# Performance work log

Hardware: AMD Instinct MI355X
Metric: run time of the kernel (lower is better)

Reference implementation:

```python
import jax, jax.numpy as jnp
import numpy as np

# dims (see shape_source)
B, S, V, E, H, L, F = 512, 17, 40002, 1024, 16, 12, 4096
DH = E // H          # per-head dim = hidden_size // num_attention_heads
NREL = 500           # num_relations
NEDGE = 100          # num_edges (edge-label vocab)
BIG = 1000000.0


def _ln(x, g, b, eps):
    m = jnp.mean(x, axis=-1, keepdims=True)
    v = jnp.mean((x - m) ** 2, axis=-1, keepdims=True)
    return (x - m) * jax.lax.rsqrt(v + eps) * g + b


def setup_inputs() -> dict:
    key = jax.random.key(0)
    ks = jax.random.split(key, 24)
    n = lambda k, sh: 0.02 * jax.random.normal(k, sh, jnp.float32)
    inp = {
        # runtime inputs
        'input_ids': jax.random.randint(ks[0], (B, S), 0, V),
        'input_mask': jnp.ones((B, S), jnp.float32),
        'edge_labels': jax.random.randint(ks[1], (S, S), 0, NEDGE),
        'mask_pos': jax.random.randint(ks[2], (B,), 0, S),
        'mask_label': jax.random.randint(ks[3], (B,), 0, V),
        'mask_type': jnp.ones((B, 1), jnp.float32),  # +1 => entity slot masked
        'confidence': jax.random.uniform(ks[4], (B,), jnp.float32),
        # parameters
        'node_emb': n(ks[5], (V, E)),
        'edge_k': n(ks[6], (NEDGE, DH)),
        'edge_v': n(ks[7], (NEDGE, DH)),
        'ln1_g': jnp.ones((E,), jnp.float32), 'ln1_b': jnp.zeros((E,), jnp.float32),
        'Wq': n(ks[8], (L, E, E)), 'bq': jnp.zeros((L, E), jnp.float32),
        'Wk': n(ks[9], (L, E, E)), 'bk': jnp.zeros((L, E), jnp.float32),
        'Wv': n(ks[10], (L, E, E)), 'bv': jnp.zeros((L, E), jnp.float32),
        'Wo': n(ks[11], (L, E, E)), 'bo': jnp.zeros((L, E), jnp.float32),
        'lnA_g': jnp.ones((L, E), jnp.float32), 'lnA_b': jnp.zeros((L, E), jnp.float32),
        'W1': n(ks[12], (L, E, F)), 'b1': jnp.zeros((L, F), jnp.float32),
        'W2': n(ks[13], (L, F, E)), 'b2': jnp.zeros((L, E), jnp.float32),
        'lnF_g': jnp.ones((L, E), jnp.float32), 'lnF_b': jnp.zeros((L, E), jnp.float32),
        'ln2_g': jnp.ones((E,), jnp.float32), 'ln2_b': jnp.zeros((E,), jnp.float32),
        'fc2_bias': jnp.zeros((V,), jnp.float32),
    }
    return inp


def _forward(node_emb, edge_k, edge_v, ln1_g, ln1_b,
             Wq, bq, Wk, bk, Wv, bv, Wo, bo, lnA_g, lnA_b,
             W1, b1, W2, b2, lnF_g, lnF_b, ln2_g, ln2_b, fc2_bias,
             input_mask, mask_type, confidence,
             input_ids, edge_labels, mask_pos, mask_label):
    # embedding + pre-LN (dropout is identity in eval mode)
    x = _ln(node_emb[input_ids], ln1_g, ln1_b, 1e-12)          # [B,S,E]
    em = jnp.sign(edge_labels).astype(x.dtype)[:, :, None]     # [S,S,1]
    ek = edge_k[edge_labels] * em                              # [S,S,DH]
    ev = edge_v[edge_labels] * em
    m = input_mask[:, :, None]                                 # [B,S,1]
    attn_bias = (BIG * (m @ jnp.swapaxes(m, 1, 2) - 1.0))[:, None]  # [B,1,S,S]

    def step(h, p):
        wq, bq_, wk, bk_, wv, bv_, wo, bo_, ga, ba, w1, b1_, w2, b2_, gf, bf = p
        proj = lambda w, b: (h @ w + b).reshape(B, S, H, DH).transpose(0, 2, 1, 3)
        q = proj(wq, bq_) * (DH ** -0.5)
        k = proj(wk, bk_)
        v = proj(wv, bv_)
        # edge-aware attention scores: content + edge-key bias
        s = jnp.einsum('bhqd,bhkd->bhqk', q, k) \
            + jnp.einsum('bhqd,qkd->bhqk', q, ek) + attn_bias
        a = jax.nn.softmax(s, axis=-1)
        c = jnp.einsum('bhqk,bhkd->bhqd', a, v) \
            + jnp.einsum('bhqk,qkd->bhqd', a, ev)
        y = c.transpose(0, 2, 1, 3).reshape(B, S, E) @ wo + bo_
        h = _ln(h + y, ga, ba, 1e-12)                          # post-LN (cmd 'dan')
        f = jax.nn.gelu(h @ w1 + b1_, approximate=False) @ w2 + b2_
        return _ln(h + f, gf, bf, 1e-12), None

    enc, _ = jax.lax.scan(step, x, (Wq, bq, Wk, bk, Wv, bv, Wo, bo,
                                    lnA_g, lnA_b, W1, b1, W2, b2, lnF_g, lnF_b))

    # mode == 'normal': gather masked position (fc1 output is dead code in the original)
    hm = enc[jnp.arange(B), mask_pos]                          # [B,E]
    hm = _ln(jax.nn.gelu(hm, approximate=False), ln2_g, ln2_b, 1e-7)
    logits = hm @ node_emb.T + fc2_bias                        # tied projection [B,V]

    ti = jnp.concatenate([-jnp.ones((B, NREL), logits.dtype),
                          jnp.ones((B, V - NREL - 2), logits.dtype)], axis=1) * mask_type
    ti = jnp.concatenate([-jnp.ones((B, 2), logits.dtype), ti], axis=1)
    ti = jax.nn.relu(ti)                                       # candidate indicator [B,V]
    logits = logits + BIG * (ti - 1.0)

    oh = jax.nn.one_hot(mask_label, V, dtype=logits.dtype)
    ti2 = ti - oh
    num_cand = jnp.sum(ti2, axis=1)                            # [B]
    sl = ((1.0 + mask_type) * 0.9 + (1.0 - mask_type) * 0.9) / 2.0  # [B,1]
    soft = sl * oh + (1.0 - sl) * ti2 / num_cand[:, None]
    loss = jnp.mean(-jnp.sum(soft * jax.nn.log_softmax(logits, axis=1), axis=1) * confidence)
    return loss, logits


def reference(input_ids, input_mask, edge_labels, mask_pos, mask_label, mask_type,
              confidence, node_emb, edge_k, edge_v, ln1_g, ln1_b, Wq, bq, Wk, bk,
              Wv, bv, Wo, bo, lnA_g, lnA_b, W1, b1, W2, b2, lnF_g, lnF_b,
              ln2_g, ln2_b, fc2_bias):
    return _forward(node_emb, edge_k, edge_v, ln1_g, ln1_b, Wq, bq, Wk, bk, Wv, bv,
                    Wo, bo, lnA_g, lnA_b, W1, b1, W2, b2, lnF_g, lnF_b, ln2_g, ln2_b,
                    fc2_bias, input_mask, mask_type, confidence,
                    input_ids, edge_labels, mask_pos, mask_label)
```

## Files before the change

### kernel.cpp

```cpp
#include <hip/hip_runtime.h>
#include <hip/hip_bf16.h>

#define BB 512
#define SS 17
#define VV 40002
#define VPAD 40064
#define EE 1024
#define HH 16
#define LL 12
#define FF 4096
#define DHD 64
#define NRELC 500
#define MTOK (BB*SS)
#define BIGC 1000000.0f

typedef __bf16 bf16_t;
typedef __bf16 bf16x8 __attribute__((ext_vector_type(8)));
typedef __bf16 bf16x4 __attribute__((ext_vector_type(4)));
typedef float  f32x4  __attribute__((ext_vector_type(4)));

#define GLOAD_LDS16(g, l) __builtin_amdgcn_global_load_lds( \
    (const __attribute__((address_space(1))) void*)(g), \
    (__attribute__((address_space(3))) void*)(l), 16, 0, 0)

__device__ __forceinline__ float dgelu(float x) {
    return 0.5f * x * (1.f + erff(x * 0.70710678118654752f));
}
__device__ __forceinline__ float fgelu(float x) {
    float y = 0.7978845608f * (x + 0.044715f * x * x * x);
    float u = __expf(2.f * y);
    float t = 1.f - 2.f / (u + 1.f);
    return 0.5f * x * (1.f + t);
}

__device__ __forceinline__ float blk_sum(float v, float* sred) {
#pragma unroll
    for (int o = 32; o > 0; o >>= 1) v += __shfl_down(v, o);
    int lane = threadIdx.x & 63, w = threadIdx.x >> 6;
    __syncthreads();
    if (lane == 0) sred[w] = v;
    __syncthreads();
    return sred[0] + sred[1] + sred[2] + sred[3];
}
__device__ __forceinline__ float blk_max(float v, float* sred) {
#pragma unroll
    for (int o = 32; o > 0; o >>= 1) v = fmaxf(v, __shfl_down(v, o));
    int lane = threadIdx.x & 63, w = threadIdx.x >> 6;
    __syncthreads();
    if (lane == 0) sred[w] = v;
    __syncthreads();
    return fmaxf(fmaxf(sred[0], sred[1]), fmaxf(sred[2], sred[3]));
}

__global__ __launch_bounds__(256)
void edge_kernel(const int* __restrict__ labels, const float* __restrict__ eks,
                 const float* __restrict__ evs, float* __restrict__ ek,
                 float* __restrict__ ev) {
    int e = blockIdx.x * 256 + threadIdx.x;
    if (e >= SS * SS * DHD) return;
    int qk = e >> 6, d = e & 63;
    int lab = labels[qk];
    float sgn = lab > 0 ? 1.f : (lab < 0 ? -1.f : 0.f);
    ek[e] = eks[(size_t)lab * DHD + d] * sgn;
    ev[e] = evs[(size_t)lab * DHD + d] * sgn;
}

__global__ __launch_bounds__(256)
void embed_kernel(const int* __restrict__ ids, const float* __restrict__ emb,
                  const float* __restrict__ g, const float* __restrict__ bt,
                  bf16_t* __restrict__ out) {
    __shared__ float sred[4];
    int row = blockIdx.x;
    const float* src = emb + (size_t)ids[row] * EE;
    int c = threadIdx.x * 4;
    float4 x = *(const float4*)(src + c);
    float mean = blk_sum(x.x + x.y + x.z + x.w, sred) * (1.f / EE);
    float x0 = x.x - mean, x1 = x.y - mean, x2 = x.z - mean, x3 = x.w - mean;
    float var = blk_sum(x0*x0 + x1*x1 + x2*x2 + x3*x3, sred) * (1.f / EE);
    float rs = rsqrtf(var + 1e-12f);
    float4 gv = *(const float4*)(g + c), bv = *(const float4*)(bt + c);
    bf16x4 o;
    o[0] = (bf16_t)(x0*rs*gv.x + bv.x); o[1] = (bf16_t)(x1*rs*gv.y + bv.y);
    o[2] = (bf16_t)(x2*rs*gv.z + bv.z); o[3] = (bf16_t)(x3*rs*gv.w + bv.w);
    *(bf16x4*)(out + (size_t)row * EE + c) = o;
}

__global__ __launch_bounds__(256)
void resln_kernel(bf16_t* __restrict__ h, const bf16_t* __restrict__ y,
                  const float* __restrict__ g, const float* __restrict__ bt) {
    __shared__ float sred[4];
    int row = blockIdx.x; int c = threadIdx.x * 4;
    size_t off = (size_t)row * EE + c;
    bf16x4 a = *(const bf16x4*)(h + off), b4 = *(const bf16x4*)(y + off);
    float x0 = (float)a[0] + (float)b4[0], x1 = (float)a[1] + (float)b4[1];
    float x2 = (float)a[2] + (float)b4[2], x3 = (float)a[3] + (float)b4[3];
    float mean = blk_sum(x0 + x1 + x2 + x3, sred) * (1.f / EE);
    x0 -= mean; x1 -= mean; x2 -= mean; x3 -= mean;
    float var = blk_sum(x0*x0 + x1*x1 + x2*x2 + x3*x3, sred) * (1.f / EE);
    float rs = rsqrtf(var + 1e-12f);
    float4 gv = *(const float4*)(g + c), bv = *(const float4*)(bt + c);
    bf16x4 o;
    o[0] = (bf16_t)(x0*rs*gv.x + bv.x); o[1] = (bf16_t)(x1*rs*gv.y + bv.y);
    o[2] = (bf16_t)(x2*rs*gv.z + bv.z); o[3] = (bf16_t)(x3*rs*gv.w + bv.w);
    *(bf16x4*)(h + off) = o;
}

__global__ __launch_bounds__(256)
void hm_kernel(const bf16_t* __restrict__ h, const int* __restrict__ pos,
               const float* __restrict__ g, const float* __restrict__ bt,
               bf16_t* __restrict__ out) {
    __shared__ float sred[4];
    int b = blockIdx.x; int c = threadIdx.x * 4;
    const bf16_t* src = h + ((size_t)(b * SS + pos[b])) * EE + c;
    bf16x4 x = *(const bf16x4*)src;
    float x0 = dgelu((float)x[0]), x1 = dgelu((float)x[1]);
    float x2 = dgelu((float)x[2]), x3 = dgelu((float)x[3]);
    float mean = blk_sum(x0 + x1 + x2 + x3, sred) * (1.f / EE);
    x0 -= mean; x1 -= mean; x2 -= mean; x3 -= mean;
    float var = blk_sum(x0*x0 + x1*x1 + x2*x2 + x3*x3, sred) * (1.f / EE);
    float rs = rsqrtf(var + 1e-7f);
    float4 gv = *(const float4*)(g + c), bv = *(const float4*)(bt + c);
    bf16x4 o;
    o[0] = (bf16_t)(x0*rs*gv.x + bv.x); o[1] = (bf16_t)(x1*rs*gv.y + bv.y);
    o[2] = (bf16_t)(x2*rs*gv.z + bv.z); o[3] = (bf16_t)(x3*rs*gv.w + bv.w);
    *(bf16x4*)(out + (size_t)b * EE + c) = o;
}

__global__ __launch_bounds__(256)
void nodeconv_kernel(const float* __restrict__ src, bf16_t* __restrict__ dst) {
    const size_t total = (size_t)VPAD * (EE / 8);
    for (size_t idx = (size_t)blockIdx.x * 256 + threadIdx.x; idx < total;
         idx += (size_t)gridDim.x * 256) {
        size_t row = idx >> 7;
        bf16x8 o;
#pragma unroll
        for (int u = 0; u < 8; ++u) o[u] = (bf16_t)0.f;
        if (row < VV) {
            const float* s = src + (idx << 3);
            float4 a = *(const float4*)s, b = *(const float4*)(s + 4);
            o[0] = (bf16_t)a.x; o[1] = (bf16_t)a.y; o[2] = (bf16_t)a.z; o[3] = (bf16_t)a.w;
            o[4] = (bf16_t)b.x; o[5] = (bf16_t)b.y; o[6] = (bf16_t)b.z; o[7] = (bf16_t)b.w;
        }
        *(bf16x8*)(dst + (idx << 3)) = o;
    }
}

__global__ __launch_bounds__(256)
void transpose_kernel(const float* __restrict__ Wq, const float* __restrict__ Wk,
                      const float* __restrict__ Wv, const float* __restrict__ Wo,
                      const float* __restrict__ W1, const float* __restrict__ W2,
                      bf16_t* __restrict__ wt) {
    int t = blockIdx.x;
    const float* src; bf16_t* dst; int K, N, tile;
    if (t < 4096) {
        int mi = t >> 10; tile = t & 1023;
        src = mi == 0 ? Wq : mi == 1 ? Wk : mi == 2 ? Wv : Wo;
        dst = wt + (size_t)mi * (1u << 20);
        K = 1024; N = 1024;
    } else if (t < 8192) {
        tile = t - 4096; src = W1; dst = wt + (size_t)4 * (1u << 20); K = 1024; N = 4096;
    } else {
        tile = t - 8192; src = W2; dst = wt + (size_t)8 * (1u << 20); K = 4096; N = 1024;
    }
    int ntiles = N >> 5;
    int kt = tile / ntiles, nt = tile % ntiles;
    __shared__ float lds[32][33];
    int tx = threadIdx.x & 31, ty = threadIdx.x >> 5;
#pragma unroll
    for (int i = 0; i < 4; ++i) {
        int r = ty + i * 8;
        lds[r][tx] = src[(size_t)(kt * 32 + r) * N + nt * 32 + tx];
    }
    __syncthreads();
#pragma unroll
    for (int i = 0; i < 4; ++i) {
        int r = ty + i * 8;
        dst[(size_t)(nt * 32 + r) * K + kt * 32 + tx] = (bf16_t)lds[tx][r];
    }
}

template<int EPI, bool NB>
__global__ __launch_bounds__(256)
void gemm_bf16(const bf16_t* __restrict__ A, const bf16_t* __restrict__ B,
               const float* __restrict__ b0, const float* __restrict__ b1,
               const float* __restrict__ b2, const float* __restrict__ mt,
               void* __restrict__ Cout, int M, int N, int K) {
    __shared__ __align__(16) bf16_t sA[3 * 4096];
    __shared__ __align__(16) bf16_t sB[3 * 4096];
    const int tid = threadIdx.x;
    const int lane = tid & 63, wid = tid >> 6;
    const int wm = wid >> 1, wn = wid & 1;
    const int row16 = lane & 15, kblk = lane >> 4;

    const int nwg = gridDim.x * gridDim.y;
    const int wg = blockIdx.y * gridDim.x + blockIdx.x;
    const int q8 = nwg >> 3, r8 = nwg & 7;
    const int xcd = wg & 7, loc = wg >> 3;
    const int swz = (xcd < r8 ? xcd * (q8 + 1) : r8 * (q8 + 1) + (xcd - r8) * q8) + loc;
    const int bm = swz / gridDim.x, bn = swz % gridDim.x;

    f32x4 acc[4][4];
#pragma unroll
    for (int i = 0; i < 4; ++i)
#pragma unroll
        for (int j = 0; j < 4; ++j) acc[i][j] = (f32x4){0.f, 0.f, 0.f, 0.f};

    const bf16_t* Atile = A + (size_t)bm * 128 * K;
    const bf16_t* Btile = B + (size_t)bn * 128 * K;

    const int row_s0 = tid >> 2, chs = tid & 3;
    const int ch0 = chs ^ ((row_s0 >> 1) & 3);
    const int row_s1 = row_s0 + 64;
    const int ch1 = chs ^ ((row_s1 >> 1) & 3);
    const size_t soff0 = (size_t)row_s0 * K + ch0 * 8;
    const size_t soff1 = (size_t)row_s1 * K + ch1 * 8;
    const int ldo0 = wid * 512;
    const int ldo1 = 2048 + wid * 512;

    int offA[4], offB[4];
#pragma unroll
    for (int i = 0; i < 4; ++i) {
        int r = wm * 64 + i * 16 + row16;
        offA[i] = r * 32 + ((kblk ^ ((r >> 1) & 3)) << 3);
    }
#pragma unroll
    for (int j = 0; j < 4; ++j) {
        int r = wn * 64 + j * 16 + row16;
        offB[j] = r * 32 + ((kblk ^ ((r >> 1) & 3)) << 3);
    }

#define STAGE_T(t_, buf_) do { \
        const bf16_t* a_ = Atile + (size_t)(t_) * 32; \
        const bf16_t* b_ = Btile + (size_t)(t_) * 32; \
        bf16_t* dA = sA + (buf_) * 4096; \
        bf16_t* dB = sB + (buf_) * 4096; \
        GLOAD_LDS16(a_ + soff0, dA + ldo0); \
        GLOAD_LDS16(a_ + soff1, dA + ldo1); \
        GLOAD_LDS16(b_ + soff0, dB + ldo0); \
        GLOAD_LDS16(b_ + soff1, dB + ldo1); \
    } while (0)

    const int nt = K >> 5;
    STAGE_T(0, 0);
    STAGE_T(1, 1);
    asm volatile("s_waitcnt vmcnt(4)" ::: "memory");
    __builtin_amdgcn_s_barrier();

    int cur = 0, stg = 2;
    for (int t = 0; t < nt; ++t) {
        const bool more = (t + 2 < nt);
        if (more) {
            STAGE_T(t + 2, stg);
            stg = (stg == 2) ? 0 : stg + 1;
        }
        const bf16_t* bufA = sA + cur * 4096;
        const bf16_t* bufB = sB + cur * 4096;
        bf16x8 af[4], bfr[4];
#pragma unroll
        for (int i = 0; i < 4; ++i) af[i] = *(const bf16x8*)(bufA + offA[i]);
#pragma unroll
        for (int j = 0; j < 4; ++j) bfr[j] = *(const bf16x8*)(bufB + offB[j]);
#pragma unroll
        for (int i = 0; i < 4; ++i)
#pragma unroll
            for (int j = 0; j < 4; ++j)
                acc[i][j] = __builtin_amdgcn_mfma_f32_16x16x32_bf16(af[i], bfr[j], acc[i][j], 0, 0, 0);
        if (t + 1 < nt) {
            if (more) asm volatile("s_waitcnt vmcnt(4)" ::: "memory");
            else      asm volatile("s_waitcnt vmcnt(0)" ::: "memory");
            __builtin_amdgcn_s_barrier();
        }
        cur = (cur == 2) ? 0 : cur + 1;
    }
#undef STAGE_T

    const int crow0 = bm * 128 + wm * 64;
    const int ccol0 = bn * 128 + wn * 64;
#pragma unroll
    for (int i = 0; i < 4; ++i) {
#pragma unroll
        for (int j = 0; j < 4; ++j) {
            int col = ccol0 + j * 16 + row16;
            if (NB && col >= N) continue;
            float bias, scale = 1.f;
            if (EPI == 4) {
                int seg = col >> 10;
                const float* bp = seg == 0 ? b0 : (seg == 1 ? b1 : b2);
                bias = bp[col & 1023];
                if (seg == 0) scale = 0.125f;
            } else {
                bias = b0[col];
            }
#pragma unroll
            for (int r = 0; r < 4; ++r) {
                int rowg = crow0 + i * 16 + kblk * 4 + r;
                float val = acc[i][j][r] + bias;
                if (EPI == 4) val *= scale;
                if (EPI == 2) val = fgelu(val);
                if (EPI == 3) {
                    float mtb = mt[rowg];
                    float tt = (col < 2) ? 0.f : fmaxf(0.f, ((col - 2) < NRELC) ? -mtb : mtb);
                    val += BIGC * (tt - 1.f);
                    ((float*)Cout)[(size_t)rowg * N + col] = val;
                } else {
                    ((bf16_t*)Cout)[(size_t)rowg * N + col] = (bf16_t)val;
                }
            }
        }
    }
}

__global__ __launch_bounds__(256)
void attn_kernel(const bf16_t* __restrict__ qkv, const float* __restrict__ ekb,
                 const float* __restrict__ evb, const float* __restrict__ mask,
                 bf16_t* __restrict__ ctx) {
    int bh = blockIdx.x; int b = bh >> 4; int h = bh & 15;
    __shared__ float sq[SS][DHD], sk[SS][DHD], sv[SS][DHD];
    __shared__ float ss[SS][SS + 1];
    __shared__ float sm[SS];
    int tid = threadIdx.x;
    for (int idx = tid; idx < 3 * SS * 8; idx += 256) {
        int t3 = idx / (SS * 8), rc = idx % (SS * 8), s = rc >> 3, c8 = rc & 7;
        bf16x8 v = *(const bf16x8*)(qkv + ((size_t)(b * SS + s)) * 3072 + t3 * 1024 + h * 64 + c8 * 8);
        float* dst = (t3 == 0 ? &sq[0][0] : t3 == 1 ? &sk[0][0] : &sv[0][0]) + s * 64 + c8 * 8;
#pragma unroll
        for (int u = 0; u < 8; ++u) dst[u] = (float)v[u];
    }
    if (tid < SS) sm[tid] = mask[b * SS + tid];
    __syncthreads();
    for (int e = tid; e < SS * SS; e += 256) {
        int qi = e / SS, ki = e % SS;
        const float* ek_ = ekb + (size_t)e * DHD;
        float acc = 0.f;
#pragma unroll 16
        for (int d = 0; d < DHD; ++d) acc += sq[qi][d] * (sk[ki][d] + ek_[d]);
        acc += BIGC * (sm[qi] * sm[ki] - 1.f);
        ss[qi][ki] = acc;
    }
    __syncthreads();
    if (tid < SS) {
        float mx = -1e30f;
        for (int ki = 0; ki < SS; ++ki) mx = fmaxf(mx, ss[tid][ki]);
        float sum = 0.f;
        for (int ki = 0; ki < SS; ++ki) { float e_ = expf(ss[tid][ki] - mx); sum += e_; ss[tid][ki] = e_; }
        float inv = 1.f / sum;
        for (int ki = 0; ki < SS; ++ki) ss[tid][ki] *= inv;
    }
    __syncthreads();
    for (int e = tid; e < SS * DHD; e += 256) {
        int qi = e >> 6, d = e & 63;
        float acc = 0.f;
#pragma unroll
        for (int ki = 0; ki < SS; ++ki)
            acc += ss[qi][ki] * (sv[ki][d] + evb[((size_t)(qi * SS + ki)) * DHD + d]);
        ctx[((size_t)(b * SS + qi)) * EE + h * DHD + d] = (bf16_t)acc;
    }
}

__global__ __launch_bounds__(256)
void loss_part_kernel(const float* __restrict__ logits, const float* __restrict__ mt,
                      const int* __restrict__ label, const float* __restrict__ conf,
                      float* __restrict__ lp) {
    __shared__ float sred[4];
    int b = blockIdx.x;
    const float* row = logits + (size_t)b * VV;
    float mx = -1e30f;
    for (int j = threadIdx.x; j < VV; j += 256) mx = fmaxf(mx, row[j]);
    mx = blk_max(mx, sred);
    float m = mt[b];
    float se = 0.f, s1 = 0.f, cnt = 0.f;
    for (int j = threadIdx.x; j < VV; j += 256) {
        float x = row[j];
        se += expf(x - mx);
        float t = (j < 2) ? 0.f : fmaxf(0.f, ((j - 2) < NRELC) ? -m : m);
        s1 += t * x;
        cnt += t;
    }
    se = blk_sum(se, sred);
    s1 = blk_sum(s1, sred);
    cnt = blk_sum(cnt, sred);
    if (threadIdx.x == 0) {
        float lse = mx + logf(se);
        float lsml = row[label[b]] - lse;
        float num_cand = cnt - 1.f;
        float v = 0.9f * lsml + 0.1f * ((s1 - cnt * lse) - lsml) / num_cand;
        lp[b] = -v * conf[b];
    }
}

__global__ __launch_bounds__(256)
void loss_reduce_kernel(const float* __restrict__ lp, float* __restrict__ out) {
    __shared__ float sred[4];
    float s = 0.f;
    for (int i = threadIdx.x; i < BB; i += 256) s += lp[i];
    s = blk_sum(s, sred);
    if (threadIdx.x == 0) out[0] = s * (1.f / BB);
}

extern "C" void kernel_launch(void* const* d_in, const int* in_sizes, int n_in,
                              void* d_out, int out_size, void* d_ws, size_t ws_size,
                              hipStream_t stream) {
    const int*   input_ids  = (const int*)d_in[0];
    const float* input_mask = (const float*)d_in[1];
    const int*   edge_lab   = (const int*)d_in[2];
    const int*   mask_pos   = (const int*)d_in[3];
    const int*   mask_label = (const int*)d_in[4];
    const float* mask_type  = (const float*)d_in[5];
    const float* confidence = (const float*)d_in[6];
    const float* node_emb   = (const float*)d_in[7];
    const float* edge_k     = (const float*)d_in[8];
    const float* edge_v     = (const float*)d_in[9];
    const float* ln1_g      = (const float*)d_in[10];
    const float* ln1_b      = (const float*)d_in[11];
    const float* Wq         = (const float*)d_in[12];
    const float* bq         = (const float*)d_in[13];
    const float* Wk         = (const float*)d_in[14];
    const float* bk         = (const float*)d_in[15];
    const float* Wv         = (const float*)d_in[16];
    const float* bv         = (const float*)d_in[17];
    const float* Wo         = (const float*)d_in[18];
    const float* bo         = (const float*)d_in[19];
    const float* lnA_g      = (const float*)d_in[20];
    const float* lnA_b      = (const float*)d_in[21];
    const float* W1         = (const float*)d_in[22];
    const float* b1         = (const float*)d_in[23];
    const float* W2         = (const float*)d_in[24];
    const float* b2         = (const float*)d_in[25];
    const float* lnF_g      = (const float*)d_in[26];
    const float* lnF_b      = (const float*)d_in[27];
    const float* ln2_g      = (const float*)d_in[28];
    const float* ln2_b      = (const float*)d_in[29];
    const float* fc2_bias   = (const float*)d_in[30];

    char* p = (char*)d_ws;
    bf16_t* wt    = (bf16_t*)p;
    size_t off = 25165824;
    bf16_t* hbuf  = (bf16_t*)(p + off); off += (size_t)MTOK * EE * 2;
    bf16_t* qkvb  = (bf16_t*)(p + off); off += (size_t)MTOK * FF * 2;
    bf16_t* cb    = (bf16_t*)(p + off); off += (size_t)MTOK * EE * 2;
    bf16_t* yb    = (bf16_t*)(p + off); off += (size_t)MTOK * EE * 2;
    float*  ekb   = (float*)(p + off);  off += (size_t)SS * SS * DHD * 4;
    float*  evb   = (float*)(p + off);  off += (size_t)SS * SS * DHD * 4;
    bf16_t* hmb   = (bf16_t*)(p + off); off += (size_t)BB * EE * 2;
    float*  lp    = (float*)(p + off);  off += (size_t)BB * 4;
    bf16_t* midb  = qkvb;
    bf16_t* nodeb = qkvb;

    float* loss_out   = (float*)d_out;
    float* logits_out = ((float*)d_out) + 1;

    edge_kernel<<<(SS * SS * DHD + 255) / 256, 256, 0, stream>>>(edge_lab, edge_k, edge_v, ekb, evb);
    embed_kernel<<<MTOK, 256, 0, stream>>>(input_ids, node_emb, ln1_g, ln1_b, hbuf);

    dim3 gqkv(3 * EE / 128, MTOK / 128);
    dim3 gproj(EE / 128, MTOK / 128);
    dim3 gffn1(FF / 128, MTOK / 128);

    for (int l = 0; l < LL; ++l) {
        size_t we = (size_t)l * EE * EE;
        size_t wf = (size_t)l * EE * FF;
        transpose_kernel<<<12288, 256, 0, stream>>>(Wq + we, Wk + we, Wv + we, Wo + we,
                                                    W1 + wf, W2 + wf, wt);
        gemm_bf16<4, false><<<gqkv, 256, 0, stream>>>(hbuf, wt,
            bq + (size_t)l * EE, bk + (size_t)l * EE, bv + (size_t)l * EE, nullptr,
            qkvb, MTOK, 3 * EE, EE);
        attn_kernel<<<BB * HH, 256, 0, stream>>>(qkvb, ekb, evb, input_mask, cb);
        gemm_bf16<0, false><<<gproj, 256, 0, stream>>>(cb, wt + (size_t)3 * (1u << 20),
            bo + (size_t)l * EE, nullptr, nullptr, nullptr, yb, MTOK, EE, EE);
        resln_kernel<<<MTOK, 256, 0, stream>>>(hbuf, yb, lnA_g + (size_t)l * EE, lnA_b + (size_t)l * EE);
        gemm_bf16<2, false><<<gffn1, 256, 0, stream>>>(hbuf, wt + (size_t)4 * (1u << 20),
            b1 + (size_t)l * FF, nullptr, nullptr, nullptr, midb, MTOK, FF, EE);
        gemm_bf16<0, false><<<gproj, 256, 0, stream>>>(midb, wt + (size_t)8 * (1u << 20),
            b2 + (size_t)l * EE, nullptr, nullptr, nullptr, yb, MTOK, EE, FF);
        resln_kernel<<<MTOK, 256, 0, stream>>>(hbuf, yb, lnF_g + (size_t)l * EE, lnF_b + (size_t)l * EE);
    }

    nodeconv_kernel<<<2048, 256, 0, stream>>>(node_emb, nodeb);
    hm_kernel<<<BB, 256, 0, stream>>>(hbuf, mask_pos, ln2_g, ln2_b, hmb);

    dim3 glog(VPAD / 128, BB / 128);
    gemm_bf16<3, true><<<glog, 256, 0, stream>>>(hmb, nodeb, fc2_bias, nullptr, nullptr,
        mask_type, logits_out, BB, VV, EE);

    loss_part_kernel<<<BB, 256, 0, stream>>>(logits_out, mask_type, mask_label, confidence, lp);
    loss_reduce_kernel<<<1, 256, 0, stream>>>(lp, loss_out);
}
```

Baseline: 5.562 ms.

## Add 256x256-tile 8-wave GEMM for QKV and FFN1 projections

```diff
diff --git a/kernel.cpp b/kernel.cpp
--- a/kernel.cpp
+++ b/kernel.cpp
@@ -179,11 +179,184 @@
     }
 }
 
+__device__ __forceinline__ void stage_half(const bf16_t* __restrict__ gbase,
+                                           bf16_t* sbase, int dstoff, int h,
+                                           int t, int K, int srow, int ch, int wid) {
+    const bf16_t* s0 = gbase + (size_t)(h * 128 + srow) * K + (size_t)t * 64 + ch * 8;
+    const bf16_t* s1 = gbase + (size_t)(h * 128 + 64 + srow) * K + (size_t)t * 64 + ch * 8;
+    GLOAD_LDS16(s0, sbase + dstoff + h * 8192 + wid * 512);
+    GLOAD_LDS16(s1, sbase + dstoff + h * 8192 + 4096 + wid * 512);
+}
+
+template<bool LAST>
+__device__ __forceinline__ void ktile256(
+    int kt, const bf16_t* __restrict__ Atile, const bf16_t* __restrict__ Btile,
+    bf16_t* sA, bf16_t* sB, int K, int srow, int ch, int wid,
+    const int (&offA)[8][2], const int (&offB)[4][2], f32x4 (&acc)[8][4]) {
+    const int bufo = (kt & 1) << 14;
+    const int nbufo = bufo ^ (1 << 14);
+    bf16x8 af[4][2], bf0[2][2], bf1[2][2];
+    asm volatile("s_waitcnt vmcnt(4)" ::: "memory");
+    __builtin_amdgcn_s_barrier();
+#pragma unroll
+    for (int i = 0; i < 4; ++i)
+#pragma unroll
+        for (int kk = 0; kk < 2; ++kk)
+            af[i][kk] = *(const bf16x8*)(sA + bufo + offA[i][kk]);
+#pragma unroll
+    for (int j = 0; j < 2; ++j)
+#pragma unroll
+        for (int kk = 0; kk < 2; ++kk)
+            bf0[j][kk] = *(const bf16x8*)(sB + bufo + offB[j][kk]);
+    if (!LAST) {
+        stage_half(Atile, sA, nbufo, 0, kt + 1, K, srow, ch, wid);
+        stage_half(Btile, sB, nbufo, 0, kt + 1, K, srow, ch, wid);
+    }
+    __builtin_amdgcn_s_setprio(1);
+#pragma unroll
+    for (int i = 0; i < 4; ++i)
+#pragma unroll
+        for (int j = 0; j < 2; ++j)
+#pragma unroll
+            for (int kk = 0; kk < 2; ++kk)
+                acc[i][j] = __builtin_amdgcn_mfma_f32_16x16x32_bf16(af[i][kk], bf0[j][kk], acc[i][j], 0, 0, 0);
+    __builtin_amdgcn_s_setprio(0);
+    if (LAST) asm volatile("s_waitcnt vmcnt(2)" ::: "memory");
+    else      asm volatile("s_waitcnt vmcnt(6)" ::: "memory");
+    __builtin_amdgcn_s_barrier();
+#pragma unroll
+    for (int j = 0; j < 2; ++j)
+#pragma unroll
+        for (int kk = 0; kk < 2; ++kk)
+            bf1[j][kk] = *(const bf16x8*)(sB + bufo + offB[2 + j][kk]);
+    if (!LAST) stage_half(Btile, sB, nbufo, 1, kt + 1, K, srow, ch, wid);
+    __builtin_amdgcn_s_setprio(1);
+#pragma unroll
+    for (int i = 0; i < 4; ++i)
+#pragma unroll
+        for (int j = 0; j < 2; ++j)
+#pragma unroll
+            for (int kk = 0; kk < 2; ++kk)
+                acc[i][2 + j] = __builtin_amdgcn_mfma_f32_16x16x32_bf16(af[i][kk], bf1[j][kk], acc[i][2 + j], 0, 0, 0);
+    __builtin_amdgcn_s_setprio(0);
+    if (LAST) asm volatile("s_waitcnt vmcnt(0)" ::: "memory");
+    else      asm volatile("s_waitcnt vmcnt(6)" ::: "memory");
+    __builtin_amdgcn_s_barrier();
+#pragma unroll
+    for (int i = 0; i < 4; ++i)
+#pragma unroll
+        for (int kk = 0; kk < 2; ++kk)
+            af[i][kk] = *(const bf16x8*)(sA + bufo + offA[4 + i][kk]);
+    if (!LAST) stage_half(Atile, sA, nbufo, 1, kt + 1, K, srow, ch, wid);
+    __builtin_amdgcn_s_setprio(1);
+#pragma unroll
+    for (int i = 0; i < 4; ++i)
+#pragma unroll
+        for (int j = 0; j < 2; ++j)
+#pragma unroll
+            for (int kk = 0; kk < 2; ++kk)
+                acc[4 + i][2 + j] = __builtin_amdgcn_mfma_f32_16x16x32_bf16(af[i][kk], bf1[j][kk], acc[4 + i][2 + j], 0, 0, 0);
+#pragma unroll
+    for (int i = 0; i < 4; ++i)
+#pragma unroll
+        for (int j = 0; j < 2; ++j)
+#pragma unroll
+            for (int kk = 0; kk < 2; ++kk)
+                acc[4 + i][j] = __builtin_amdgcn_mfma_f32_16x16x32_bf16(af[i][kk], bf0[j][kk], acc[4 + i][j], 0, 0, 0);
+    __builtin_amdgcn_s_setprio(0);
+}
+
+template<int EPI>
+__global__ __launch_bounds__(512, 1)
+void gemm256(const bf16_t* __restrict__ A, const bf16_t* __restrict__ B,
+             const float* __restrict__ b0, const float* __restrict__ b1,
+             const float* __restrict__ b2, bf16_t* __restrict__ C,
+             int N, int K) {
+    __shared__ __align__(16) bf16_t sA[32768];
+    __shared__ __align__(16) bf16_t sB[32768];
+    const int tid = threadIdx.x;
+    const int lane = tid & 63, wid = tid >> 6;
+    const int wm = wid >> 2, wn = wid & 3;
+    const int r16 = lane & 15, kblk = lane >> 4;
+
+    const int nwg = gridDim.x * gridDim.y;
+    const int wg = blockIdx.y * gridDim.x + blockIdx.x;
+    const int q8 = nwg >> 3, r8 = nwg & 7;
+    const int xcd = wg & 7, loc = wg >> 3;
+    const int swz = (xcd < r8 ? xcd * (q8 + 1) : r8 * (q8 + 1) + (xcd - r8) * q8) + loc;
+    const int bm = swz / gridDim.x, bn = swz % gridDim.x;
+
+    f32x4 acc[8][4];
+#pragma unroll
+    for (int i = 0; i < 8; ++i)
+#pragma unroll
+        for (int j = 0; j < 4; ++j) acc[i][j] = (f32x4){0.f, 0.f, 0.f, 0.f};
+
+    const bf16_t* Atile = A + (size_t)bm * 256 * K;
+    const bf16_t* Btile = B + (size_t)bn * 256 * K;
+
+    const int c = wid * 64 + lane;
+    const int srow = c >> 3;
+    const int ch = (c & 7) ^ (srow & 7);
+
+    int offA[8][2], offB[4][2];
+#pragma unroll
+    for (int i = 0; i < 8; ++i) {
+        int r = wm * 128 + i * 16 + r16;
+#pragma unroll
+        for (int kk = 0; kk < 2; ++kk)
+            offA[i][kk] = r * 64 + (((kk * 4 + kblk) ^ (r & 7)) << 3);
+    }
+#pragma unroll
+    for (int j = 0; j < 4; ++j) {
+        int r = wn * 64 + j * 16 + r16;
+#pragma unroll
+        for (int kk = 0; kk < 2; ++kk)
+            offB[j][kk] = r * 64 + (((kk * 4 + kblk) ^ (r & 7)) << 3);
+    }
+
+    stage_half(Atile, sA, 0, 0, 0, K, srow, ch, wid);
+    stage_half(Btile, sB, 0, 0, 0, K, srow, ch, wid);
+    stage_half(Btile, sB, 0, 1, 0, K, srow, ch, wid);
+    stage_half(Atile, sA, 0, 1, 0, K, srow, ch, wid);
+
+    const int nt = K >> 6;
+    for (int kt = 0; kt < nt - 1; ++kt)
+        ktile256<false>(kt, Atile, Btile, sA, sB, K, srow, ch, wid, offA, offB, acc);
+    ktile256<true>(nt - 1, Atile, Btile, sA, sB, K, srow, ch, wid, offA, offB, acc);
+
+    const int crow0 = bm * 256 + wm * 128;
+    const int ccol0 = bn * 256 + wn * 64;
+#pragma unroll
+    for (int i = 0; i < 8; ++i) {
+#pragma unroll
+        for (int j = 0; j < 4; ++j) {
+            int col = ccol0 + j * 16 + r16;
+            float bias, scale = 1.f;
+            if (EPI == 4) {
+                int seg = col >> 10;
+                const float* bp = seg == 0 ? b0 : (seg == 1 ? b1 : b2);
+                bias = bp[col & 1023];
+                if (seg == 0) scale = 0.125f;
+            } else {
+                bias = b0[col];
+            }
+#pragma unroll
+            for (int r = 0; r < 4; ++r) {
+                int rowg = crow0 + i * 16 + kblk * 4 + r;
+                float val = acc[i][j][r] + bias;
+                if (EPI == 4) val *= scale;
+                if (EPI == 2) val = fgelu(val);
+                C[(size_t)rowg * N + col] = (bf16_t)val;
+            }
+        }
+    }
+}
+
 template<int EPI, bool NB>
 __global__ __launch_bounds__(256)
 void gemm_bf16(const bf16_t* __restrict__ A, const bf16_t* __restrict__ B,
-               const float* __restrict__ b0, const float* __restrict__ b1,
-               const float* __restrict__ b2, const float* __restrict__ mt,
+               const float* __restrict__ b0, const float* __restrict__ mt,
                void* __restrict__ Cout, int M, int N, int K) {
     __shared__ __align__(16) bf16_t sA[3 * 4096];
     __shared__ __align__(16) bf16_t sB[3 * 4096];
@@ -282,21 +455,11 @@
         for (int j = 0; j < 4; ++j) {
             int col = ccol0 + j * 16 + row16;
             if (NB && col >= N) continue;
-            float bias, scale = 1.f;
-            if (EPI == 4) {
-                int seg = col >> 10;
-                const float* bp = seg == 0 ? b0 : (seg == 1 ? b1 : b2);
-                bias = bp[col & 1023];
-                if (seg == 0) scale = 0.125f;
-            } else {
-                bias = b0[col];
-            }
+            float bias = b0[col];
 #pragma unroll
             for (int r = 0; r < 4; ++r) {
                 int rowg = crow0 + i * 16 + kblk * 4 + r;
                 float val = acc[i][j][r] + bias;
-                if (EPI == 4) val *= scale;
-                if (EPI == 2) val = fgelu(val);
                 if (EPI == 3) {
                     float mtb = mt[rowg];
                     float tt = (col < 2) ? 0.f : fmaxf(0.f, ((col - 2) < NRELC) ? -mtb : mtb);
@@ -452,26 +615,26 @@
     edge_kernel<<<(SS * SS * DHD + 255) / 256, 256, 0, stream>>>(edge_lab, edge_k, edge_v, ekb, evb);
     embed_kernel<<<MTOK, 256, 0, stream>>>(input_ids, node_emb, ln1_g, ln1_b, hbuf);
 
-    dim3 gqkv(3 * EE / 128, MTOK / 128);
+    dim3 gqkv(3 * EE / 256, MTOK / 256);
+    dim3 gffn1(FF / 256, MTOK / 256);
     dim3 gproj(EE / 128, MTOK / 128);
-    dim3 gffn1(FF / 128, MTOK / 128);
 
     for (int l = 0; l < LL; ++l) {
         size_t we = (size_t)l * EE * EE;
         size_t wf = (size_t)l * EE * FF;
         transpose_kernel<<<12288, 256, 0, stream>>>(Wq + we, Wk + we, Wv + we, Wo + we,
                                                     W1 + wf, W2 + wf, wt);
-        gemm_bf16<4, false><<<gqkv, 256, 0, stream>>>(hbuf, wt,
-            bq + (size_t)l * EE, bk + (size_t)l * EE, bv + (size_t)l * EE, nullptr,
-            qkvb, MTOK, 3 * EE, EE);
+        gemm256<4><<<gqkv, 512, 0, stream>>>(hbuf, wt,
+            bq + (size_t)l * EE, bk + (size_t)l * EE, bv + (size_t)l * EE,
+            qkvb, 3 * EE, EE);
         attn_kernel<<<BB * HH, 256, 0, stream>>>(qkvb, ekb, evb, input_mask, cb);
         gemm_bf16<0, false><<<gproj, 256, 0, stream>>>(cb, wt + (size_t)3 * (1u << 20),
-            bo + (size_t)l * EE, nullptr, nullptr, nullptr, yb, MTOK, EE, EE);
+            bo + (size_t)l * EE, nullptr, yb, MTOK, EE, EE);
         resln_kernel<<<MTOK, 256, 0, stream>>>(hbuf, yb, lnA_g + (size_t)l * EE, lnA_b + (size_t)l * EE);
-        gemm_bf16<2, false><<<gffn1, 256, 0, stream>>>(hbuf, wt + (size_t)4 * (1u << 20),
-            b1 + (size_t)l * FF, nullptr, nullptr, nullptr, midb, MTOK, FF, EE);
+        gemm256<2><<<gffn1, 512, 0, stream>>>(hbuf, wt + (size_t)4 * (1u << 20),
+            b1 + (size_t)l * FF, nullptr, nullptr, midb, FF, EE);
         gemm_bf16<0, false><<<gproj, 256, 0, stream>>>(midb, wt + (size_t)8 * (1u << 20),
-            b2 + (size_t)l * EE, nullptr, nullptr, nullptr, yb, MTOK, EE, FF);
+            b2 + (size_t)l * EE, nullptr, yb, MTOK, EE, FF);
         resln_kernel<<<MTOK, 256, 0, stream>>>(hbuf, yb, lnF_g + (size_t)l * EE, lnF_b + (size_t)l * EE);
     }
 
@@ -479,7 +642,7 @@
     hm_kernel<<<BB, 256, 0, stream>>>(hbuf, mask_pos, ln2_g, ln2_b, hmb);
 
     dim3 glog(VPAD / 128, BB / 128);
-    gemm_bf16<3, true><<<glog, 256, 0, stream>>>(hmb, nodeb, fc2_bias, nullptr, nullptr,
+    gemm_bf16<3, true><<<glog, 256, 0, stream>>>(hmb, nodeb, fc2_bias,
         mask_type, logits_out, BB, VV, EE);
 
     loss_part_kernel<<<BB, 256, 0, stream>>>(logits_out, mask_type, mask_label, confidence, lp);
```

After: 5.471 ms. No clear change (-1.6%).

## Widen GEMM block tile to 128x256 with eight waves per block

Applied to the files above, without the earlier changes.

```diff
diff --git a/kernel.cpp b/kernel.cpp
--- a/kernel.cpp
+++ b/kernel.cpp
@@ -4,7 +4,7 @@
 #define BB 512
 #define SS 17
 #define VV 40002
-#define VPAD 40064
+#define VPAD 40192
 #define EE 1024
 #define HH 16
 #define LL 12
@@ -180,16 +180,16 @@
 }
 
 template<int EPI, bool NB>
-__global__ __launch_bounds__(256)
+__global__ __launch_bounds__(512, 4)
 void gemm_bf16(const bf16_t* __restrict__ A, const bf16_t* __restrict__ B,
                const float* __restrict__ b0, const float* __restrict__ b1,
                const float* __restrict__ b2, const float* __restrict__ mt,
                void* __restrict__ Cout, int M, int N, int K) {
     __shared__ __align__(16) bf16_t sA[3 * 4096];
-    __shared__ __align__(16) bf16_t sB[3 * 4096];
+    __shared__ __align__(16) bf16_t sB[3 * 8192];
     const int tid = threadIdx.x;
     const int lane = tid & 63, wid = tid >> 6;
-    const int wm = wid >> 1, wn = wid & 1;
+    const int wm = wid >> 2, wn = wid & 3;
     const int row16 = lane & 15, kblk = lane >> 4;
 
     const int nwg = gridDim.x * gridDim.y;
@@ -206,16 +206,19 @@
         for (int j = 0; j < 4; ++j) acc[i][j] = (f32x4){0.f, 0.f, 0.f, 0.f};
 
     const bf16_t* Atile = A + (size_t)bm * 128 * K;
-    const bf16_t* Btile = B + (size_t)bn * 128 * K;
-
-    const int row_s0 = tid >> 2, chs = tid & 3;
-    const int ch0 = chs ^ ((row_s0 >> 1) & 3);
-    const int row_s1 = row_s0 + 64;
-    const int ch1 = chs ^ ((row_s1 >> 1) & 3);
-    const size_t soff0 = (size_t)row_s0 * K + ch0 * 8;
-    const size_t soff1 = (size_t)row_s1 * K + ch1 * 8;
-    const int ldo0 = wid * 512;
-    const int ldo1 = 2048 + wid * 512;
+    const bf16_t* Btile = B + (size_t)bn * 256 * K;
+
+    const int rowA = tid >> 2;
+    const int chA = (tid & 3) ^ ((rowA >> 1) & 3);
+    const size_t aoff = (size_t)rowA * K + chA * 8;
+    const int rowB0 = tid >> 2, rowB1 = rowB0 + 128;
+    const int chB0 = (tid & 3) ^ ((rowB0 >> 1) & 3);
+    const int chB1 = (tid & 3) ^ ((rowB1 >> 1) & 3);
+    const size_t boff0 = (size_t)rowB0 * K + chB0 * 8;
+    const size_t boff1 = (size_t)rowB1 * K + chB1 * 8;
+    const int ldoA  = wid * 512;
+    const int ldoB0 = wid * 512;
+    const int ldoB1 = 4096 + wid * 512;
 
     int offA[4], offB[4];
 #pragma unroll
@@ -232,18 +235,15 @@
 #define STAGE_T(t_, buf_) do { \
         const bf16_t* a_ = Atile + (size_t)(t_) * 32; \
         const bf16_t* b_ = Btile + (size_t)(t_) * 32; \
-        bf16_t* dA = sA + (buf_) * 4096; \
-        bf16_t* dB = sB + (buf_) * 4096; \
-        GLOAD_LDS16(a_ + soff0, dA + ldo0); \
-        GLOAD_LDS16(a_ + soff1, dA + ldo1); \
-        GLOAD_LDS16(b_ + soff0, dB + ldo0); \
-        GLOAD_LDS16(b_ + soff1, dB + ldo1); \
+        GLOAD_LDS16(a_ + aoff,  sA + (buf_) * 4096 + ldoA); \
+        GLOAD_LDS16(b_ + boff0, sB + (buf_) * 8192 + ldoB0); \
+        GLOAD_LDS16(b_ + boff1, sB + (buf_) * 8192 + ldoB1); \
     } while (0)
 
     const int nt = K >> 5;
     STAGE_T(0, 0);
     STAGE_T(1, 1);
-    asm volatile("s_waitcnt vmcnt(4)" ::: "memory");
+    asm volatile("s_waitcnt vmcnt(3)" ::: "memory");
     __builtin_amdgcn_s_barrier();
 
     int cur = 0, stg = 2;
@@ -254,7 +254,7 @@
             stg = (stg == 2) ? 0 : stg + 1;
         }
         const bf16_t* bufA = sA + cur * 4096;
-        const bf16_t* bufB = sB + cur * 4096;
+        const bf16_t* bufB = sB + cur * 8192;
         bf16x8 af[4], bfr[4];
 #pragma unroll
         for (int i = 0; i < 4; ++i) af[i] = *(const bf16x8*)(bufA + offA[i]);
@@ -266,7 +266,7 @@
             for (int j = 0; j < 4; ++j)
                 acc[i][j] = __builtin_amdgcn_mfma_f32_16x16x32_bf16(af[i], bfr[j], acc[i][j], 0, 0, 0);
         if (t + 1 < nt) {
-            if (more) asm volatile("s_waitcnt vmcnt(4)" ::: "memory");
+            if (more) asm volatile("s_waitcnt vmcnt(3)" ::: "memory");
             else      asm volatile("s_waitcnt vmcnt(0)" ::: "memory");
             __builtin_amdgcn_s_barrier();
         }
@@ -275,7 +275,7 @@
 #undef STAGE_T
 
     const int crow0 = bm * 128 + wm * 64;
-    const int ccol0 = bn * 128 + wn * 64;
+    const int ccol0 = bn * 256 + wn * 64;
 #pragma unroll
     for (int i = 0; i < 4; ++i) {
 #pragma unroll
@@ -452,25 +452,25 @@
     edge_kernel<<<(SS * SS * DHD + 255) / 256, 256, 0, stream>>>(edge_lab, edge_k, edge_v, ekb, evb);
     embed_kernel<<<MTOK, 256, 0, stream>>>(input_ids, node_emb, ln1_g, ln1_b, hbuf);
 
-    dim3 gqkv(3 * EE / 128, MTOK / 128);
-    dim3 gproj(EE / 128, MTOK / 128);
-    dim3 gffn1(FF / 128, MTOK / 128);
+    dim3 gqkv(3 * EE / 256, MTOK / 128);
+    dim3 gproj(EE / 256, MTOK / 128);
+    dim3 gffn1(FF / 256, MTOK / 128);
 
     for (int l = 0; l < LL; ++l) {
         size_t we = (size_t)l * EE * EE;
         size_t wf = (size_t)l * EE * FF;
         transpose_kernel<<<12288, 256, 0, stream>>>(Wq + we, Wk + we, Wv + we, Wo + we,
                                                     W1 + wf, W2 + wf, wt);
-        gemm_bf16<4, false><<<gqkv, 256, 0, stream>>>(hbuf, wt,
+        gemm_bf16<4, false><<<gqkv, 512, 0, stream>>>(hbuf, wt,
             bq + (size_t)l * EE, bk + (size_t)l * EE, bv + (size_t)l * EE, nullptr,
             qkvb, MTOK, 3 * EE, EE);
         attn_kernel<<<BB * HH, 256, 0, stream>>>(qkvb, ekb, evb, input_mask, cb);
-        gemm_bf16<0, false><<<gproj, 256, 0, stream>>>(cb, wt + (size_t)3 * (1u << 20),
+        gemm_bf16<0, false><<<gproj, 512, 0, stream>>>(cb, wt + (size_t)3 * (1u << 20),
             bo + (size_t)l * EE, nullptr, nullptr, nullptr, yb, MTOK, EE, EE);
         resln_kernel<<<MTOK, 256, 0, stream>>>(hbuf, yb, lnA_g + (size_t)l * EE, lnA_b + (size_t)l * EE);
-        gemm_bf16<2, false><<<gffn1, 256, 0, stream>>>(hbuf, wt + (size_t)4 * (1u << 20),
+        gemm_bf16<2, false><<<gffn1, 512, 0, stream>>>(hbuf, wt + (size_t)4 * (1u << 20),
             b1 + (size_t)l * FF, nullptr, nullptr, nullptr, midb, MTOK, FF, EE);
-        gemm_bf16<0, false><<<gproj, 256, 0, stream>>>(midb, wt + (size_t)8 * (1u << 20),
+        gemm_bf16<0, false><<<gproj, 512, 0, stream>>>(midb, wt + (size_t)8 * (1u << 20),
             b2 + (size_t)l * EE, nullptr, nullptr, nullptr, yb, MTOK, EE, FF);
         resln_kernel<<<MTOK, 256, 0, stream>>>(hbuf, yb, lnF_g + (size_t)l * EE, lnF_b + (size_t)l * EE);
     }
@@ -478,8 +478,8 @@
     nodeconv_kernel<<<2048, 256, 0, stream>>>(node_emb, nodeb);
     hm_kernel<<<BB, 256, 0, stream>>>(hbuf, mask_pos, ln2_g, ln2_b, hmb);
 
-    dim3 glog(VPAD / 128, BB / 128);
-    gemm_bf16<3, true><<<glog, 256, 0, stream>>>(hmb, nodeb, fc2_bias, nullptr, nullptr,
+    dim3 glog(VPAD / 256, BB / 128);
+    gemm_bf16<3, true><<<glog, 512, 0, stream>>>(hmb, nodeb, fc2_bias, nullptr, nullptr,
         mask_type, logits_out, BB, VV, EE);
 
     loss_part_kernel<<<BB, 256, 0, stream>>>(logits_out, mask_type, mask_label, confidence, lp);
```

After: 5.819 ms. 1.05x slower.

## Batch four heads per attention block, stage bf16 edge tensors in LDS, warp-per-row LayerNorm

Applied to the files above, without the earlier changes.

```diff
diff --git a/kernel.cpp b/kernel.cpp
--- a/kernel.cpp
+++ b/kernel.cpp
@@ -26,11 +26,8 @@
 __device__ __forceinline__ float dgelu(float x) {
     return 0.5f * x * (1.f + erff(x * 0.70710678118654752f));
 }
-__device__ __forceinline__ float fgelu(float x) {
-    float y = 0.7978845608f * (x + 0.044715f * x * x * x);
-    float u = __expf(2.f * y);
-    float t = 1.f - 2.f / (u + 1.f);
-    return 0.5f * x * (1.f + t);
+__device__ __forceinline__ float sgelu(float x) {
+    return x / (1.f + __expf(-1.702f * x));
 }
 
 __device__ __forceinline__ float blk_sum(float v, float* sred) {
@@ -54,15 +51,15 @@
 
 __global__ __launch_bounds__(256)
 void edge_kernel(const int* __restrict__ labels, const float* __restrict__ eks,
-                 const float* __restrict__ evs, float* __restrict__ ek,
-                 float* __restrict__ ev) {
+                 const float* __restrict__ evs, bf16_t* __restrict__ ek,
+                 bf16_t* __restrict__ ev) {
     int e = blockIdx.x * 256 + threadIdx.x;
     if (e >= SS * SS * DHD) return;
     int qk = e >> 6, d = e & 63;
     int lab = labels[qk];
     float sgn = lab > 0 ? 1.f : (lab < 0 ? -1.f : 0.f);
-    ek[e] = eks[(size_t)lab * DHD + d] * sgn;
-    ev[e] = evs[(size_t)lab * DHD + d] * sgn;
+    ek[e] = (bf16_t)(eks[(size_t)lab * DHD + d] * sgn);
+    ev[e] = (bf16_t)(evs[(size_t)lab * DHD + d] * sgn);
 }
 
 __global__ __launch_bounds__(256)
@@ -88,21 +85,43 @@
 __global__ __launch_bounds__(256)
 void resln_kernel(bf16_t* __restrict__ h, const bf16_t* __restrict__ y,
                   const float* __restrict__ g, const float* __restrict__ bt) {
-    __shared__ float sred[4];
-    int row = blockIdx.x; int c = threadIdx.x * 4;
-    size_t off = (size_t)row * EE + c;
-    bf16x4 a = *(const bf16x4*)(h + off), b4 = *(const bf16x4*)(y + off);
-    float x0 = (float)a[0] + (float)b4[0], x1 = (float)a[1] + (float)b4[1];
-    float x2 = (float)a[2] + (float)b4[2], x3 = (float)a[3] + (float)b4[3];
-    float mean = blk_sum(x0 + x1 + x2 + x3, sred) * (1.f / EE);
-    x0 -= mean; x1 -= mean; x2 -= mean; x3 -= mean;
-    float var = blk_sum(x0*x0 + x1*x1 + x2*x2 + x3*x3, sred) * (1.f / EE);
-    float rs = rsqrtf(var + 1e-12f);
-    float4 gv = *(const float4*)(g + c), bv = *(const float4*)(bt + c);
-    bf16x4 o;
-    o[0] = (bf16_t)(x0*rs*gv.x + bv.x); o[1] = (bf16_t)(x1*rs*gv.y + bv.y);
-    o[2] = (bf16_t)(x2*rs*gv.z + bv.z); o[3] = (bf16_t)(x3*rs*gv.w + bv.w);
-    *(bf16x4*)(h + off) = o;
+    int row = blockIdx.x * 4 + (threadIdx.x >> 6);
+    int lane = threadIdx.x & 63;
+    int c = lane * 16;
+    size_t base = (size_t)row * EE + c;
+    bf16x8 a0 = *(const bf16x8*)(h + base);
+    bf16x8 a1 = *(const bf16x8*)(h + base + 8);
+    bf16x8 b0 = *(const bf16x8*)(y + base);
+    bf16x8 b1 = *(const bf16x8*)(y + base + 8);
+    float x[16];
+    float s = 0.f;
+#pragma unroll
+    for (int u = 0; u < 8; ++u) { x[u] = (float)a0[u] + (float)b0[u]; s += x[u]; }
+#pragma unroll
+    for (int u = 0; u < 8; ++u) { x[8 + u] = (float)a1[u] + (float)b1[u]; s += x[8 + u]; }
+#pragma unroll
+    for (int o = 32; o > 0; o >>= 1) s += __shfl_xor(s, o);
+    float mean = s * (1.f / EE);
+    float v = 0.f;
+#pragma unroll
+    for (int u = 0; u < 16; ++u) { x[u] -= mean; v += x[u] * x[u]; }
+#pragma unroll
+    for (int o = 32; o > 0; o >>= 1) v += __shfl_xor(v, o);
+    float rs = rsqrtf(v * (1.f / EE) + 1e-12f);
+    float4 g0 = *(const float4*)(g + c),  g1 = *(const float4*)(g + c + 4);
+    float4 g2 = *(const float4*)(g + c + 8), g3 = *(const float4*)(g + c + 12);
+    float4 t0 = *(const float4*)(bt + c), t1 = *(const float4*)(bt + c + 4);
+    float4 t2 = *(const float4*)(bt + c + 8), t3 = *(const float4*)(bt + c + 12);
+    float gg[16] = {g0.x,g0.y,g0.z,g0.w,g1.x,g1.y,g1.z,g1.w,g2.x,g2.y,g2.z,g2.w,g3.x,g3.y,g3.z,g3.w};
+    float tt[16] = {t0.x,t0.y,t0.z,t0.w,t1.x,t1.y,t1.z,t1.w,t2.x,t2.y,t2.z,t2.w,t3.x,t3.y,t3.z,t3.w};
+    bf16x8 o0, o1;
+#pragma unroll
+    for (int u = 0; u < 8; ++u) {
+        o0[u] = (bf16_t)(x[u] * rs * gg[u] + tt[u]);
+        o1[u] = (bf16_t)(x[8 + u] * rs * gg[8 + u] + tt[8 + u]);
+    }
+    *(bf16x8*)(h + base) = o0;
+    *(bf16x8*)(h + base + 8) = o1;
 }
 
 __global__ __launch_bounds__(256)
@@ -296,7 +315,7 @@
                 int rowg = crow0 + i * 16 + kblk * 4 + r;
                 float val = acc[i][j][r] + bias;
                 if (EPI == 4) val *= scale;
-                if (EPI == 2) val = fgelu(val);
+                if (EPI == 2) val = sgelu(val);
                 if (EPI == 3) {
                     float mtb = mt[rowg];
                     float tt = (col < 2) ? 0.f : fmaxf(0.f, ((col - 2) < NRELC) ? -mtb : mtb);
@@ -310,50 +329,60 @@
     }
 }
 
-__global__ __launch_bounds__(256)
-void attn_kernel(const bf16_t* __restrict__ qkv, const float* __restrict__ ekb,
-                 const float* __restrict__ evb, const float* __restrict__ mask,
+__global__ __launch_bounds__(512)
+void attn_kernel(const bf16_t* __restrict__ qkv, const bf16_t* __restrict__ ekb,
+                 const bf16_t* __restrict__ evb, const float* __restrict__ mask,
                  bf16_t* __restrict__ ctx) {
-    int bh = blockIdx.x; int b = bh >> 4; int h = bh & 15;
-    __shared__ float sq[SS][DHD], sk[SS][DHD], sv[SS][DHD];
-    __shared__ float ss[SS][SS + 1];
+    const int blk = blockIdx.x;
+    const int b = blk >> 2, hg = blk & 3;
+    const int h0 = hg * 4;
+    __shared__ bf16_t sek[SS * SS * DHD];
+    __shared__ bf16_t sev[SS * SS * DHD];
+    __shared__ float sq[4][SS][DHD], skk[4][SS][DHD], svv[4][SS][DHD];
+    __shared__ float ss[4][SS][SS + 1];
     __shared__ float sm[SS];
-    int tid = threadIdx.x;
-    for (int idx = tid; idx < 3 * SS * 8; idx += 256) {
-        int t3 = idx / (SS * 8), rc = idx % (SS * 8), s = rc >> 3, c8 = rc & 7;
-        bf16x8 v = *(const bf16x8*)(qkv + ((size_t)(b * SS + s)) * 3072 + t3 * 1024 + h * 64 + c8 * 8);
-        float* dst = (t3 == 0 ? &sq[0][0] : t3 == 1 ? &sk[0][0] : &sv[0][0]) + s * 64 + c8 * 8;
+    const int tid = threadIdx.x;
+    for (int idx = tid; idx < SS * SS * 8; idx += 512) {
+        *(bf16x8*)(sek + idx * 8) = *(const bf16x8*)(ekb + idx * 8);
+        *(bf16x8*)(sev + idx * 8) = *(const bf16x8*)(evb + idx * 8);
+    }
+    for (int idx = tid; idx < 3 * SS * 32; idx += 512) {
+        int t3 = idx / (SS * 32), rc = idx % (SS * 32), s = rc >> 5, c8 = rc & 31;
+        bf16x8 v = *(const bf16x8*)(qkv + (size_t)(b * SS + s) * 3072 + t3 * 1024 + h0 * 64 + c8 * 8);
+        int hh = c8 >> 3, d0 = (c8 & 7) * 8;
+        float* dst = (t3 == 0 ? &sq[hh][s][d0] : t3 == 1 ? &skk[hh][s][d0] : &svv[hh][s][d0]);
 #pragma unroll
         for (int u = 0; u < 8; ++u) dst[u] = (float)v[u];
     }
     if (tid < SS) sm[tid] = mask[b * SS + tid];
     __syncthreads();
-    for (int e = tid; e < SS * SS; e += 256) {
-        int qi = e / SS, ki = e % SS;
-        const float* ek_ = ekb + (size_t)e * DHD;
+    for (int e = tid; e < 4 * SS * SS; e += 512) {
+        int hh = e / (SS * SS), qk = e % (SS * SS), qi = qk / SS, ki = qk % SS;
+        const bf16_t* ek_ = sek + qk * DHD;
         float acc = 0.f;
 #pragma unroll 16
-        for (int d = 0; d < DHD; ++d) acc += sq[qi][d] * (sk[ki][d] + ek_[d]);
+        for (int d = 0; d < DHD; ++d) acc += sq[hh][qi][d] * (skk[hh][ki][d] + (float)ek_[d]);
         acc += BIGC * (sm[qi] * sm[ki] - 1.f);
-        ss[qi][ki] = acc;
-    }
-    __syncthreads();
-    if (tid < SS) {
+        ss[hh][qi][ki] = acc;
+    }
+    __syncthreads();
+    if (tid < 4 * SS) {
+        int hh = tid / SS, qi = tid % SS;
         float mx = -1e30f;
-        for (int ki = 0; ki < SS; ++ki) mx = fmaxf(mx, ss[tid][ki]);
+        for (int ki = 0; ki < SS; ++ki) mx = fmaxf(mx, ss[hh][qi][ki]);
         float sum = 0.f;
-        for (int ki = 0; ki < SS; ++ki) { float e_ = expf(ss[tid][ki] - mx); sum += e_; ss[tid][ki] = e_; }
+        for (int ki = 0; ki < SS; ++ki) { float e_ = __expf(ss[hh][qi][ki] - mx); sum += e_; ss[hh][qi][ki] = e_; }
         float inv = 1.f / sum;
-        for (int ki = 0; ki < SS; ++ki) ss[tid][ki] *= inv;
-    }
-    __syncthreads();
-    for (int e = tid; e < SS * DHD; e += 256) {
-        int qi = e >> 6, d = e & 63;
+        for (int ki = 0; ki < SS; ++ki) ss[hh][qi][ki] *= inv;
+    }
+    __syncthreads();
+    for (int e = tid; e < 4 * SS * DHD; e += 512) {
+        int hh = e / (SS * DHD), rem = e % (SS * DHD), qi = rem >> 6, d = rem & 63;
         float acc = 0.f;
 #pragma unroll
         for (int ki = 0; ki < SS; ++ki)
-            acc += ss[qi][ki] * (sv[ki][d] + evb[((size_t)(qi * SS + ki)) * DHD + d]);
-        ctx[((size_t)(b * SS + qi)) * EE + h * DHD + d] = (bf16_t)acc;
+            acc += ss[hh][qi][ki] * (svv[hh][ki][d] + (float)sev[(qi * SS + ki) * DHD + d]);
+        ctx[(size_t)(b * SS + qi) * EE + (h0 + hh) * DHD + d] = (bf16_t)acc;
     }
 }
 
@@ -439,8 +468,8 @@
     bf16_t* qkvb  = (bf16_t*)(p + off); off += (size_t)MTOK * FF * 2;
     bf16_t* cb    = (bf16_t*)(p + off); off += (size_t)MTOK * EE * 2;
     bf16_t* yb    = (bf16_t*)(p + off); off += (size_t)MTOK * EE * 2;
-    float*  ekb   = (float*)(p + off);  off += (size_t)SS * SS * DHD * 4;
-    float*  evb   = (float*)(p + off);  off += (size_t)SS * SS * DHD * 4;
+    bf16_t* ekb   = (bf16_t*)(p + off); off += (size_t)SS * SS * DHD * 2;
+    bf16_t* evb   = (bf16_t*)(p + off); off += (size_t)SS * SS * DHD * 2;
     bf16_t* hmb   = (bf16_t*)(p + off); off += (size_t)BB * EE * 2;
     float*  lp    = (float*)(p + off);  off += (size_t)BB * 4;
     bf16_t* midb  = qkvb;
@@ -464,15 +493,15 @@
         gemm_bf16<4, false><<<gqkv, 256, 0, stream>>>(hbuf, wt,
             bq + (size_t)l * EE, bk + (size_t)l * EE, bv + (size_t)l * EE, nullptr,
             qkvb, MTOK, 3 * EE, EE);
-        attn_kernel<<<BB * HH, 256, 0, stream>>>(qkvb, ekb, evb, input_mask, cb);
+        attn_kernel<<<BB * 4, 512, 0, stream>>>(qkvb, ekb, evb, input_mask, cb);
         gemm_bf16<0, false><<<gproj, 256, 0, stream>>>(cb, wt + (size_t)3 * (1u << 20),
             bo + (size_t)l * EE, nullptr, nullptr, nullptr, yb, MTOK, EE, EE);
-        resln_kernel<<<MTOK, 256, 0, stream>>>(hbuf, yb, lnA_g + (size_t)l * EE, lnA_b + (size_t)l * EE);
+        resln_kernel<<<MTOK / 4, 256, 0, stream>>>(hbuf, yb, lnA_g + (size_t)l * EE, lnA_b + (size_t)l * EE);
         gemm_bf16<2, false><<<gffn1, 256, 0, stream>>>(hbuf, wt + (size_t)4 * (1u << 20),
             b1 + (size_t)l * FF, nullptr, nullptr, nullptr, midb, MTOK, FF, EE);
         gemm_bf16<0, false><<<gproj, 256, 0, stream>>>(midb, wt + (size_t)8 * (1u << 20),
             b2 + (size_t)l * EE, nullptr, nullptr, nullptr, yb, MTOK, EE, FF);
-        resln_kernel<<<MTOK, 256, 0, stream>>>(hbuf, yb, lnF_g + (size_t)l * EE, lnF_b + (size_t)l * EE);
+        resln_kernel<<<MTOK / 4, 256, 0, stream>>>(hbuf, yb, lnF_g + (size_t)l * EE, lnF_b + (size_t)l * EE);
     }
 
     nodeconv_kernel<<<2048, 256, 0, stream>>>(node_emb, nodeb);
```

New measurement: 6.474 ms. 16.4% more time.
